# Performance work log

Measured on AMD Instinct MI355X. Metric: run time of the kernel, lower is better.

Reference implementation:

```python
import jax, jax.numpy as jnp
import numpy as np

B, S, D, H = 2, 4096, 1024, 16
HD = D // H
KCONV = 4


def _rmsnorm(x, scale, eps=1e-6):
    return x * jax.lax.rsqrt(jnp.mean(x * x, axis=-1, keepdims=True) + eps) * scale


def _l2norm(x, eps=1e-6):
    return x * jax.lax.rsqrt(jnp.sum(x * x, axis=-1, keepdims=True) + eps)


def _causal_dwconv_silu(x, w):
    # x: [B,S,D], w: [D,K] depthwise taps (tap K-1 multiplies x[t])
    k = w.shape[1]
    s = x.shape[1]
    xp = jnp.pad(x, ((0, 0), (k - 1, 0), (0, 0)))
    out = sum(xp[:, i:i + s, :] * w[:, i] for i in range(k))
    return jax.nn.silu(out)


def _p20_scan(x, decay_log, theta):
    # BLOCK_DIAGONAL_2 rotary-state linear recurrence: channels paired into
    # complex state, s_t = a * s_{t-1} + u_t with a = exp(-exp(decay_log) + i*theta).
    b, s, d = x.shape
    xc = x.reshape(b, s, d // 2, 2)
    u = jax.lax.complex(xc[..., 0], xc[..., 1])  # [B,S,D/2]
    a = jnp.exp(-jnp.exp(decay_log)) * jnp.exp(1j * theta)  # [D/2] complex, |a|<1

    def step(carry, u_t):
        st = carry * a + u_t
        return st, st

    _, ys = jax.lax.scan(step, jnp.zeros((b, d // 2), u.dtype), jnp.swapaxes(u, 0, 1))
    ys = jnp.swapaxes(ys, 0, 1)  # [B,S,D/2]
    return jnp.stack([ys.real, ys.imag], axis=-1).reshape(b, s, d)


def _gated_delta_rule(q, k, v, g, beta):
    # q,k,v: [B,S,H,Dh]; g,beta: [B,S,H]. State S: [B,H,K,V].
    scale = q.shape[-1] ** -0.5
    q = _l2norm(q)
    k = _l2norm(k)
    qt, kt, vt = (jnp.moveaxis(t, 1, 0) for t in (q, k, v))
    gt, bt = (jnp.moveaxis(t, 1, 0) for t in (g, beta))
    s0 = jnp.zeros((q.shape[0], q.shape[2], q.shape[3], v.shape[3]), v.dtype)

    def step(state, inp):
        q_t, k_t, v_t, g_t, b_t = inp
        state = state * jnp.exp(g_t)[..., None, None]
        v_err = (v_t - jnp.einsum('bhkv,bhk->bhv', state, k_t)) * b_t[..., None]
        state = state + jnp.einsum('bhk,bhv->bhkv', k_t, v_err)
        o_t = jnp.einsum('bhkv,bhk->bhv', state, q_t) * scale
        return state, o_t

    _, o = jax.lax.scan(step, s0, (qt, kt, vt, gt, bt))
    return jnp.moveaxis(o, 0, 1)  # [B,S,H,V]


def setup_inputs() -> dict:
    key = jax.random.key(0)
    ks = jax.random.split(key, 16)
    w = lambda k, shp, s=0.02: (jax.random.normal(k, shp, jnp.float32) * s)
    ctrl_out = 3 * D + 2 * H + D  # q,k,v,decay,beta,output_gate
    ctrl_b = jnp.concatenate([
        jnp.zeros((3 * D,), jnp.float32),
        jnp.full((H,), 1.5, jnp.float32),       # decay bias
        jnp.full((H,), -2.0, jnp.float32),      # beta bias
        jnp.full((D,), -1.5, jnp.float32),      # output gate bias
    ])
    # depthwise conv init: delta at last tap + small noise
    def conv_w(k):
        base = jnp.zeros((D, KCONV), jnp.float32).at[:, -1].set(1.0)
        return base + w(k, (D, KCONV), 0.02)
    return {
        'hidden': jax.random.normal(ks[0], (B, S, D), jnp.float32),
        'p20_decay_log': w(ks[1], (D // 2,), 1.0),
        'p20_theta': jax.random.uniform(ks[2], (D // 2,), jnp.float32, 0.0, 2.0 * np.pi),
        'ctrl_W': w(ks[3], (D, ctrl_out)),
        'ctrl_b': ctrl_b,
        'p20c_W': w(ks[4], (D, 3 * D), 0.001),  # 0.05-scaled init
        'qconv_w': conv_w(ks[5]),
        'kconv_w': conv_w(ks[6]),
        'vconv_w': conv_w(ks[7]),
        'mnorm_scale': jnp.ones((HD,), jnp.float32),
        'vnorm_scale': jnp.ones((D,), jnp.float32),
        'ramp_logit': jnp.full((D,), -4.595, jnp.float32),  # logit(0.01)
        'out_W': w(ks[8], (2 * D, D), 0.02),
        'out_b': jnp.zeros((D,), jnp.float32),
    }


def reference(hidden, p20_decay_log, p20_theta, ctrl_W, ctrl_b, p20c_W,
              qconv_w, kconv_w, vconv_w, mnorm_scale, vnorm_scale,
              ramp_logit, out_W, out_b):
    b, s, d = hidden.shape
    # P20 vector-state side channel
    p20_read = _p20_scan(hidden, p20_decay_log, p20_theta)
    normed_p20 = _rmsnorm(p20_read, vnorm_scale)
    p20_q, p20_k, p20_v = jnp.split(normed_p20 @ p20c_W, 3, axis=-1)
    ramp = jax.nn.sigmoid(ramp_logit)  # [D]
    # packed control projection
    ctrl = hidden @ ctrl_W + ctrl_b
    q_in, k_in, v_in, dec_in, beta_in, gate_in = jnp.split(
        ctrl, np.cumsum([d, d, d, H, H]).tolist(), axis=-1)
    # causal depthwise conv + SiLU
    q_in = _causal_dwconv_silu(q_in, qconv_w)
    k_in = _causal_dwconv_silu(k_in, kconv_w)
    v_in = _causal_dwconv_silu(v_in, vconv_w)
    # P20-conditioned heads
    queries = (q_in + ramp * p20_q).reshape(b, s, H, HD)
    keys = (k_in + ramp * p20_k).reshape(b, s, H, HD)
    values = (v_in + ramp * p20_v).reshape(b, s, H, HD)
    g = jax.nn.log_sigmoid(dec_in.astype(jnp.float32)).astype(hidden.dtype)  # [B,S,H]
    beta = jax.nn.sigmoid(beta_in)
    reads = _gated_delta_rule(queries, keys, values, g, beta)
    normed_reads = _rmsnorm(reads, mnorm_scale).reshape(b, s, d)
    fused = jnp.concatenate([normed_reads, normed_p20], axis=-1)
    projected = fused @ out_W + out_b
    return jax.nn.sigmoid(gate_in) * projected
```

## Files before the change

### kernel.cpp

```cpp
#include <hip/hip_runtime.h>
#include <hip/hip_bf16.h>
#include <stdint.h>

#define SEQ  4096
#define NH   16
#define HD   64

typedef __attribute__((ext_vector_type(8))) short bf16x8;
typedef __attribute__((ext_vector_type(4))) float f32x4;

__device__ __forceinline__ float bf2f(unsigned short u){
  union{unsigned u;float f;} v; v.u = ((unsigned)u)<<16; return v.f;
}
__device__ __forceinline__ unsigned short f2bf(float f){
  union{float f;unsigned u;} v; v.f=f;
  return (unsigned short)((v.u + 0x7fffu + ((v.u>>16)&1u))>>16);
}
__device__ __forceinline__ float sigm(float x){ return 1.f/(1.f+__expf(-x)); }
__device__ __forceinline__ f32x4 mfma16(bf16x8 a, bf16x8 b, f32x4 c){
  return __builtin_amdgcn_mfma_f32_16x16x32_bf16(a,b,c,0,0,0);
}
__device__ __forceinline__ void gll16(const void* g, void* l){
  __builtin_amdgcn_global_load_lds((const __attribute__((address_space(1))) void*)g,
                                   (__attribute__((address_space(3))) void*)l, 16, 0, 0);
}

__global__ void k_fill(float* __restrict__ p, float v, long n){
  long i = (long)blockIdx.x*blockDim.x + threadIdx.x;
  long stride = (long)gridDim.x*blockDim.x;
  for (; i<n; i+=stride) p[i] = v;
}

__global__ void k_cvt_bf16(const float* __restrict__ in, unsigned short* __restrict__ out){
  long i = ((long)blockIdx.x*256 + threadIdx.x)*4;
  float4 v = *(const float4*)(in+i);
  ushort4 o; o.x=f2bf(v.x); o.y=f2bf(v.y); o.z=f2bf(v.z); o.w=f2bf(v.w);
  *(ushort4*)(out+i) = o;
}

__global__ void k_transpose(const float* __restrict__ in, unsigned short* __restrict__ out,
                            int R, int Cin, int Cpad){
  __shared__ float t[32][33];
  int cb = blockIdx.x*32, rb = blockIdx.y*32;
  int tx = threadIdx.x & 31, ty = threadIdx.x >> 5;
  for (int k=0;k<32;k+=8){
    int r = rb+ty+k, c = cb+tx;
    t[ty+k][tx] = (c<Cin) ? in[(long)r*Cin + c] : 0.f;
  }
  __syncthreads();
  for (int k=0;k<32;k+=8){
    int c = cb+ty+k, r = rb+tx;
    if (c<Cpad) out[(long)c*R + r] = f2bf(t[tx][ty+k]);
  }
}

#define FOR16(F) F(0,0) F(0,1) F(0,2) F(0,3) F(1,0) F(1,1) F(1,2) F(1,3) \
                 F(2,0) F(2,1) F(2,2) F(2,3) F(3,0) F(3,1) F(3,2) F(3,3)
#define FOR4(F) F(0) F(1) F(2) F(3)
#define ACC(i,j) Ac##i##j

#define GEMM_CORE(A_,lda_,Bt_,ldb_,K_)                                         \
  __shared__ unsigned short Ab[3][4096];                                       \
  __shared__ unsigned short Bb[3][4096];                                       \
  const int tid=threadIdx.x, wid=tid>>6, l=tid&63;                             \
  const long m0=(long)blockIdx.y*128, n0=(long)blockIdx.x*128;                 \
  const int nk=(K_)>>5;                                                        \
  const int wm=(wid>>1)*64, wn=(wid&1)*64;                                     \
  const int srow0 = tid>>2;                                                    \
  const int schunk = (((tid&3) ^ ((tid>>2)&3))<<3);                            \
  const unsigned short* gA0 = (A_) + (m0+srow0)*(lda_) + schunk;               \
  const unsigned short* gA1 = (A_) + (m0+64+srow0)*(lda_) + schunk;            \
  const unsigned short* gB0 = (Bt_) + (n0+srow0)*(ldb_) + schunk;              \
  const unsigned short* gB1 = (Bt_) + (n0+64+srow0)*(ldb_) + schunk;           \
  const int ldst0 = tid*16, ldst1 = 4096 + tid*16;                             \
  f32x4 Ac00={0.f,0.f,0.f,0.f};                                                \
  f32x4 Ac01=Ac00,Ac02=Ac00,Ac03=Ac00,Ac10=Ac00,Ac11=Ac00,Ac12=Ac00,           \
        Ac13=Ac00,Ac20=Ac00,Ac21=Ac00,Ac22=Ac00,Ac23=Ac00,Ac30=Ac00,           \
        Ac31=Ac00,Ac32=Ac00,Ac33=Ac00;                                         \
  gll16(gA0, (char*)&Ab[0][0]+ldst0); gll16(gA1, (char*)&Ab[0][0]+ldst1);      \
  gll16(gB0, (char*)&Bb[0][0]+ldst0); gll16(gB1, (char*)&Bb[0][0]+ldst1);      \
  gA0+=32; gA1+=32; gB0+=32; gB1+=32;                                          \
  gll16(gA0, (char*)&Ab[1][0]+ldst0); gll16(gA1, (char*)&Ab[1][0]+ldst1);      \
  gll16(gB0, (char*)&Bb[1][0]+ldst0); gll16(gB1, (char*)&Bb[1][0]+ldst1);      \
  gA0+=32; gA1+=32; gB0+=32; gB1+=32;                                          \
  int rb=0, sb=2;                                                              \
  const int sxor = (l&3)<<4;                                                   \
  const int rao0 = (wm+(l&15))*64 + (((l>>4)<<4) ^ sxor);                      \
  const int rbo0 = (wn+(l&15))*64 + (((l>>4)<<4) ^ sxor);                      \
  for (int kt=0; kt<nk; ++kt){                                                 \
    if (kt+1<nk) { asm volatile("s_waitcnt vmcnt(4)" ::: "memory"); }          \
    else         { asm volatile("s_waitcnt vmcnt(0)" ::: "memory"); }          \
    __builtin_amdgcn_sched_barrier(0);                                         \
    __builtin_amdgcn_s_barrier();                                              \
    __builtin_amdgcn_sched_barrier(0);                                         \
    if (kt+2<nk){                                                              \
      gll16(gA0, (char*)&Ab[sb][0]+ldst0); gll16(gA1, (char*)&Ab[sb][0]+ldst1);\
      gll16(gB0, (char*)&Bb[sb][0]+ldst0); gll16(gB1, (char*)&Bb[sb][0]+ldst1);\
      gA0+=32; gA1+=32; gB0+=32; gB1+=32;                                      \
    }                                                                          \
    const char* Apt=(const char*)&Ab[rb][0];                                   \
    const char* Bpt=(const char*)&Bb[rb][0];                                   \
    bf16x8 af0=*(const bf16x8*)(Apt+rao0);      bf16x8 bf0=*(const bf16x8*)(Bpt+rbo0);      \
    bf16x8 af1=*(const bf16x8*)(Apt+rao0+1024); bf16x8 bf1=*(const bf16x8*)(Bpt+rbo0+1024); \
    bf16x8 af2=*(const bf16x8*)(Apt+rao0+2048); bf16x8 bf2=*(const bf16x8*)(Bpt+rbo0+2048); \
    bf16x8 af3=*(const bf16x8*)(Apt+rao0+3072); bf16x8 bf3=*(const bf16x8*)(Bpt+rbo0+3072); \
    __builtin_amdgcn_s_setprio(1);                                             \
    Ac00=mfma16(af0,bf0,Ac00); Ac01=mfma16(af0,bf1,Ac01);                      \
    Ac02=mfma16(af0,bf2,Ac02); Ac03=mfma16(af0,bf3,Ac03);                      \
    Ac10=mfma16(af1,bf0,Ac10); Ac11=mfma16(af1,bf1,Ac11);                      \
    Ac12=mfma16(af1,bf2,Ac12); Ac13=mfma16(af1,bf3,Ac13);                      \
    Ac20=mfma16(af2,bf0,Ac20); Ac21=mfma16(af2,bf1,Ac21);                      \
    Ac22=mfma16(af2,bf2,Ac22); Ac23=mfma16(af2,bf3,Ac23);                      \
    Ac30=mfma16(af3,bf0,Ac30); Ac31=mfma16(af3,bf1,Ac31);                      \
    Ac32=mfma16(af3,bf2,Ac32); Ac33=mfma16(af3,bf3,Ac33);                      \
    __builtin_amdgcn_s_setprio(0);                                             \
    rb = (rb==2)?0:rb+1; sb = (sb==2)?0:sb+1;                                  \
  }

__global__ __launch_bounds__(256,2) void k_gemm(
  const unsigned short* __restrict__ A, int lda,
  const unsigned short* __restrict__ Bt, int ldb,
  unsigned short* Cb, float* Cf, int ldc,
  int K, int Nvalid,
  const float* __restrict__ bias,
  const unsigned short* __restrict__ gate, int gld)
{
  GEMM_CORE(A, lda, Bt, ldb, K)
#define EPI_GEN(mi,ni) {                                                       \
  const int gn=(int)n0+wn+ni*16+(l&15);                                        \
  if (gn<Nvalid){                                                              \
    _Pragma("unroll") for(int r=0;r<4;r++){                                    \
      const long gm=m0+wm+mi*16+((l>>4)<<2)+r;                                 \
      float v=ACC(mi,ni)[r];                                                   \
      if(bias) v+=bias[gn];                                                    \
      if(gate) v*=bf2f(gate[gm*gld+gn]);                                       \
      if(Cb) Cb[gm*ldc+gn]=f2bf(v); else Cf[gm*ldc+gn]=v; } } }
  FOR16(EPI_GEN)
#undef EPI_GEN
}

__global__ __launch_bounds__(256,2) void k_gemm_ctrl(
  const unsigned short* __restrict__ A, int lda,
  const unsigned short* __restrict__ Bt, int ldb,
  unsigned short* __restrict__ ctrl,
  float* __restrict__ gbuf, float* __restrict__ bbuf,
  unsigned short* __restrict__ gateb,
  const float* __restrict__ bias)
{
  GEMM_CORE(A, lda, Bt, ldb, 1024)
#define EPI_CTRL(mi,ni) {                                                      \
  const int gn=(int)n0+wn+ni*16+(l&15);                                        \
  if (gn<4128){                                                                \
    const float bs=bias[gn];                                                   \
    _Pragma("unroll") for(int r=0;r<4;r++){                                    \
      const long gm=m0+wm+mi*16+((l>>4)<<2)+r;                                 \
      float v=ACC(mi,ni)[r]+bs;                                                \
      if (gn<3072)      ctrl[gm*3072+gn]=f2bf(v);                              \
      else if (gn<3088) gbuf[gm*16+(gn-3072)]=                                 \
                          (v>=0.f)?-log1pf(__expf(-v)):(v-log1pf(__expf(v)));  \
      else if (gn<3104) bbuf[gm*16+(gn-3088)]=sigm(v);                         \
      else              gateb[gm*1024+(gn-3104)]=f2bf(sigm(v)); } } }
  FOR16(EPI_CTRL)
#undef EPI_CTRL
}

__global__ __launch_bounds__(256,2) void k_gemm_qkv(
  const unsigned short* __restrict__ A, int lda,
  const unsigned short* __restrict__ Bt, int ldb,
  const float* __restrict__ ramp,
  unsigned short* __restrict__ Qb, unsigned short* __restrict__ Kb,
  unsigned short* __restrict__ Vb)
{
  GEMM_CORE(A, lda, Bt, ldb, 1024)
  const int seg = (int)((n0 + wn) >> 10);
  unsigned short* Ob = (seg==0)?Qb:((seg==1)?Kb:Vb);
  const int dc0=((int)n0+wn+0*16+(l&15))&1023; const float sr0=sigm(ramp[dc0]);
  const int dc1=((int)n0+wn+1*16+(l&15))&1023; const float sr1=sigm(ramp[dc1]);
  const int dc2=((int)n0+wn+2*16+(l&15))&1023; const float sr2=sigm(ramp[dc2]);
  const int dc3=((int)n0+wn+3*16+(l&15))&1023; const float sr3=sigm(ramp[dc3]);
#define EPI_QKV(mi) {                                                          \
  _Pragma("unroll") for(int r=0;r<4;r++){                                      \
    const long gm=m0+wm+mi*16+((l>>4)<<2)+r;                                   \
    float v0=bf2f(Ob[gm*1024+dc0])+sr0*ACC(mi,0)[r];                           \
    float v1=bf2f(Ob[gm*1024+dc1])+sr1*ACC(mi,1)[r];                           \
    float v2=bf2f(Ob[gm*1024+dc2])+sr2*ACC(mi,2)[r];                           \
    float v3=bf2f(Ob[gm*1024+dc3])+sr3*ACC(mi,3)[r];                           \
    if (seg<2){                                                                \
      float ss=v0*v0+v1*v1+v2*v2+v3*v3;                                        \
      ss+=__shfl_xor(ss,1); ss+=__shfl_xor(ss,2);                              \
      ss+=__shfl_xor(ss,4); ss+=__shfl_xor(ss,8);                              \
      float rs=rsqrtf(ss+1e-6f); v0*=rs; v1*=rs; v2*=rs; v3*=rs; }             \
    Ob[gm*1024+dc0]=f2bf(v0); Ob[gm*1024+dc1]=f2bf(v1);                        \
    Ob[gm*1024+dc2]=f2bf(v2); Ob[gm*1024+dc3]=f2bf(v3); } }
  FOR4(EPI_QKV)
#undef EPI_QKV
}

__global__ void k_scan1(const float* __restrict__ hidden, const float* __restrict__ dlog,
                        const float* __restrict__ theta, float2* __restrict__ finals){
  int idx = blockIdx.x*256 + threadIdx.x;
  int ch = idx & 511; int chunk = (idx>>9) & 63; int b = idx>>15;
  float e = __expf(dlog[ch]); float r = __expf(-e);
  float th = theta[ch]; float ar = r*__cosf(th), ai = r*__sinf(th);
  const float2* src = (const float2*)hidden + ((long)b*SEQ + chunk*64)*512 + ch;
  float sr=0.f, si=0.f;
  for (int j=0;j<64;j++){
    float2 u = src[(long)j*512];
    float nr = sr*ar - si*ai + u.x;
    si = sr*ai + si*ar + u.y; sr = nr;
  }
  finals[idx] = make_float2(sr,si);
}
__global__ void k_scan2(const float* __restrict__ dlog, const float* __restrict__ theta,
                        const float2* __restrict__ finals, float2* __restrict__ carry, int nb){
  int idx = blockIdx.x*256+threadIdx.x; if (idx>=nb*512) return;
  int ch = idx & 511, b = idx>>9;
  float e = __expf(dlog[ch]); float r64 = __expf(-64.f*e);
  float ang = fmodf(64.f*theta[ch], 6.2831853071795864f);
  float cr = r64*__cosf(ang), ci = r64*__sinf(ang);
  float pr=0.f, pi=0.f;
  for (int c=0;c<64;c++){
    long o = ((long)b*64 + c)*512 + ch;
    carry[o] = make_float2(pr,pi);
    float2 f = finals[o];
    float nr = pr*cr - pi*ci + f.x;
    pi = pr*ci + pi*cr + f.y; pr = nr;
  }
}
__global__ void k_scan3(const float* __restrict__ hidden, const float* __restrict__ dlog,
                        const float* __restrict__ theta, const float2* __restrict__ carry,
                        unsigned short* __restrict__ p20){
  int idx = blockIdx.x*256 + threadIdx.x;
  int ch = idx & 511; int chunk = (idx>>9) & 63; int b = idx>>15;
  float e = __expf(dlog[ch]); float r = __expf(-e);
  float th = theta[ch]; float ar = r*__cosf(th), ai = r*__sinf(th);
  long toff = (long)b*SEQ + chunk*64;
  const float2* src = (const float2*)hidden + toff*512 + ch;
  unsigned short* dst = p20 + toff*1024 + 2*ch;
  float2 c0 = carry[idx];
  float sr=c0.x, si=c0.y;
  for (int j=0;j<64;j++){
    float2 u = src[(long)j*512];
    float nr = sr*ar - si*ai + u.x;
    si = sr*ai + si*ar + u.y; sr = nr;
    ushort2 o; o.x=f2bf(sr); o.y=f2bf(si);
    *(ushort2*)(dst + (long)j*1024) = o;
  }
}

__global__ __launch_bounds__(256) void k_rms_p20(const unsigned short* __restrict__ p20,
                        const float* __restrict__ vns, unsigned short* __restrict__ fused){
  long t = blockIdx.x;
  int d = threadIdx.x*4;
  ushort4 xu = *(const ushort4*)(p20 + t*1024 + d);
  float x0=bf2f(xu.x), x1=bf2f(xu.y), x2=bf2f(xu.z), x3=bf2f(xu.w);
  float ss = x0*x0 + x1*x1 + x2*x2 + x3*x3;
  for (int o=1;o<64;o<<=1) ss += __shfl_xor(ss, o);
  __shared__ float red[4];
  if ((threadIdx.x&63)==0) red[threadIdx.x>>6] = ss;
  __syncthreads();
  ss = red[0]+red[1]+red[2]+red[3];
  float rs = rsqrtf(ss*(1.f/1024.f) + 1e-6f);
  float4 s4 = *(const float4*)(vns + d);
  ushort4 o4;
  o4.x = f2bf(x0*rs*s4.x); o4.y = f2bf(x1*rs*s4.y);
  o4.z = f2bf(x2*rs*s4.z); o4.w = f2bf(x3*rs*s4.w);
  *(ushort4*)(fused + t*2048 + 1024 + d) = o4;
}

__global__ __launch_bounds__(256) void k_conv(const unsigned short* __restrict__ ctrl,
   const float* __restrict__ qw, const float* __restrict__ kw, const float* __restrict__ vw,
   unsigned short* __restrict__ Q, unsigned short* __restrict__ Kb, unsigned short* __restrict__ Vb){
  __shared__ unsigned short pan[19][256];
  int panel = blockIdx.x;
  int tb = blockIdx.y;
  int b = tb >> 8; int s0 = (tb & 255) * 16;
  int seg = panel >> 2; int d = (panel & 3)*256 + threadIdx.x;
  int c0 = panel*256;
  long base = (long)b*SEQ*3072;
  for (int rr=0; rr<19; rr++){
    int s = s0 - 3 + rr;
    pan[rr][threadIdx.x] = (s>=0) ? ctrl[base + (long)s*3072 + c0 + threadIdx.x] : (unsigned short)0;
  }
  __syncthreads();
  const float* cw = (seg==0)?qw:((seg==1)?kw:vw);
  float w0=cw[d*4], w1=cw[d*4+1], w2=cw[d*4+2], w3=cw[d*4+3];
  unsigned short* Ob = (seg==0)?Q:((seg==1)?Kb:Vb);
  for (int tk=0; tk<16; tk++){
    long t = (long)b*SEQ + s0 + tk;
    float x = bf2f(pan[tk][threadIdx.x])*w0 + bf2f(pan[tk+1][threadIdx.x])*w1
            + bf2f(pan[tk+2][threadIdx.x])*w2 + bf2f(pan[tk+3][threadIdx.x])*w3;
    x = x * sigm(x);
    Ob[t*1024 + d] = f2bf(x);
  }
}

__global__ __launch_bounds__(64,2) void k_phase1(
    const unsigned short* __restrict__ Kg, const unsigned short* __restrict__ Vg,
    const float* __restrict__ g, const float* __restrict__ beta,
    unsigned short* __restrict__ uvT, unsigned short* __restrict__ Wrm,
    unsigned short* __restrict__ Mc, unsigned short* __restrict__ BcT){
  __shared__ unsigned short Kc[64*64];
  __shared__ unsigned short Vc[64*64];
  __shared__ float Af[64*64];
  __shared__ unsigned short uTb[64*72];
  __shared__ unsigned short wTb[64*72];
  __shared__ float Gs[64], betl[64], bgam[64], decC[64];

  int bid = blockIdx.x; int bh = bid>>6, c = bid&63;
  int blocal = bh>>4, h = bh&15;
  long t0 = (long)blocal*SEQ + c*64;
  int l = threadIdx.x;
  long cbase = (long)bid*4096;

  float G = g[(t0+l)*16 + h];
  for (int o=1;o<64;o<<=1){ float n = __shfl_up(G,o); if (l>=o) G += n; }
  float bl = beta[(t0+l)*16+h];
  Gs[l]=G; betl[l]=bl; bgam[l]=bl*__expf(G);
  float G63 = __shfl(G,63);
  decC[l] = __expf(G63 - G);
  float GamC = __expf(G63);

  for (int it=0; it<8; it++){
    int bo = it*1024 + l*16;
    int row = bo>>7, bib = bo&127;
    int sb2 = bib ^ ((row&7)<<4);
    gll16(Kg + (t0+row)*1024 + h*64 + (sb2>>1),  (char*)Kc + bo);
    gll16(Vg + (t0+row)*1024 + h*64 + (bib>>1), (char*)Vc + bo);
  }
  __syncthreads();

  bf16x8 kf[2][4];
  {
    int rr = l&15;
    #pragma unroll
    for (int t=0;t<4;t++)
      #pragma unroll
      for (int h2=0;h2<2;h2++){
        int row = t*16 + rr;
        int byt = row*128 + ((h2*64 + (l>>4)*16) ^ ((row&7)<<4));
        kf[h2][t] = *(const bf16x8*)((const char*)Kc + byt);
      }
  }
  #pragma unroll
  for (int ti=0;ti<4;ti++){
    #pragma unroll
    for (int tj=0;tj<4;tj++){
      f32x4 a = {0.f,0.f,0.f,0.f};
      a = mfma16(kf[0][ti], kf[0][tj], a);
      a = mfma16(kf[1][ti], kf[1][tj], a);
      int j = tj*16 + (l&15);
      float Gj = Gs[j];
      #pragma unroll
      for (int r=0;r<4;r++){
        int i = ti*16 + ((l>>4)<<2) + r;
        Af[i*64+j] = (j<i) ? betl[i]*a[r]*__expf(Gs[i]-Gj) : 0.f;
      }
    }
  }
  __syncthreads();

  float ww[64];
  {
    float uu[64];
    #pragma unroll
    for (int i=0;i<64;i++){
      float ua = betl[i]*bf2f(Vc[i*64 + l]);
      float wa = bgam[i]*bf2f(*(const unsigned short*)((const char*)Kc + i*128 + ((2*l) ^ ((i&7)<<4))));
      #pragma unroll
      for (int j=0;j<i;j++){
        float av = Af[i*64+j];
        ua -= av*uu[j];
        wa -= av*ww[j];
      }
      uu[i] = ua; ww[i] = wa;
    }
    #pragma unroll
    for (int i=0;i<64;i+=4){
      short4 pu, pw;
      pu.x=(short)f2bf(uu[i]);   pu.y=(short)f2bf(uu[i+1]);
      pu.z=(short)f2bf(uu[i+2]); pu.w=(short)f2bf(uu[i+3]);
      pw.x=(short)f2bf(ww[i]);   pw.y=(short)f2bf(ww[i+1]);
      pw.z=(short)f2bf(ww[i+2]); pw.w=(short)f2bf(ww[i+3]);
      *(short4*)&uTb[l*72+i] = pu;
      *(short4*)&wTb[l*72+i] = pw;
    }
  }
  __syncthreads();

  unsigned short* KTp = (unsigned short*)Af;
  for (int j=0;j<64;j++){
    float kv = bf2f(*(const unsigned short*)((const char*)Kc + j*128 + ((2*l) ^ ((j&7)<<4))));
    *(unsigned short*)((char*)KTp + l*128 + ((2*j) ^ ((l&7)<<4))) = f2bf(decC[j]*kv);
  }
  __syncthreads();

  auto ldfragKT = [&](int t, int h2)->bf16x8{
    int row = t*16 + (l&15);
    int byt = row*128 + ((h2*64 + (l>>4)*16) ^ ((row&7)<<4));
    return *(const bf16x8*)((const char*)KTp + byt);
  };
  auto ldfrag72 = [&](const unsigned short* base, int nrow, int h2)->bf16x8{
    return *(const bf16x8*)(base + nrow*72 + h2*32 + ((l>>4)<<3));
  };

  #pragma unroll
  for (int to=0; to<4; to++){
    bf16x8 a0 = ldfragKT(to,0), a1 = ldfragKT(to,1);
    #pragma unroll
    for (int tn=0; tn<4; tn++){
      f32x4 accv = {0.f,0.f,0.f,0.f};
      accv = mfma16(a0, ldfrag72(wTb, tn*16+(l&15), 0), accv);
      accv = mfma16(a1, ldfrag72(wTb, tn*16+(l&15), 1), accv);
      int col = tn*16 + (l&15);
      #pragma unroll
      for (int r=0;r<4;r++){
        int row = to*16 + ((l>>4)<<2) + r;
        Mc[cbase + row*64 + col] = f2bf(((row==col)? GamC : 0.f) - accv[r]);
      }
    }
    #pragma unroll
    for (int tv=0; tv<4; tv++){
      f32x4 accv = {0.f,0.f,0.f,0.f};
      accv = mfma16(a0, ldfrag72(uTb, tv*16+(l&15), 0), accv);
      accv = mfma16(a1, ldfrag72(uTb, tv*16+(l&15), 1), accv);
      int v = tv*16 + (l&15);
      int k0 = to*16 + ((l>>4)<<2);
      short4 p;
      p.x=(short)f2bf(accv[0]); p.y=(short)f2bf(accv[1]);
      p.z=(short)f2bf(accv[2]); p.w=(short)f2bf(accv[3]);
      *(short4*)&BcT[cbase + v*64 + k0] = p;
    }
  }

  #pragma unroll
  for (int rr=0; rr<64; rr++){
    uvT[cbase + rr*64 + l] = uTb[rr*72 + l];
    Wrm[cbase + rr*64 + l] = f2bf(ww[rr]);
  }
}

__global__ __launch_bounds__(64,2) void k_phase2(
    const unsigned short* __restrict__ Mc, const unsigned short* __restrict__ BcT,
    unsigned short* __restrict__ Sst){
  __shared__ unsigned short ST[64*64];
  int bh = blockIdx.x; int l = threadIdx.x;
  f32x4 acc[4][4];
  { f32x4 z = {0.f,0.f,0.f,0.f};
    #pragma unroll
    for (int i=0;i<4;i++)
      #pragma unroll
      for (int j=0;j<4;j++) acc[i][j]=z; }

  for (int c=0;c<64;c++){
    long cbase = ((long)bh*64 + c)*4096;
    #pragma unroll
    for (int ti=0;ti<4;ti++){
      #pragma unroll
      for (int tj=0;tj<4;tj++){
        int v = tj*16 + (l&15);
        int kd0 = ti*16 + ((l>>4)<<2);
        short4 p;
        p.x=(short)f2bf(acc[ti][tj][0]); p.y=(short)f2bf(acc[ti][tj][1]);
        p.z=(short)f2bf(acc[ti][tj][2]); p.w=(short)f2bf(acc[ti][tj][3]);
        *(short4*)&Sst[cbase + v*64 + kd0] = p;
        *(short4*)((char*)ST + v*128 + ((2*kd0) ^ ((v&7)<<4))) = p;
      }
    }
    __syncthreads();
    bf16x8 mf[2][4];
    #pragma unroll
    for (int ti=0;ti<4;ti++){
      int row = ti*16 + (l&15);
      mf[0][ti] = *(const bf16x8*)(Mc + cbase + row*64 + (l>>4)*8);
      mf[1][ti] = *(const bf16x8*)(Mc + cbase + row*64 + 32 + (l>>4)*8);
    }
    #pragma unroll
    for (int ti=0;ti<4;ti++)
      #pragma unroll
      for (int tj=0;tj<4;tj++){
        short4 bv = *(const short4*)&BcT[cbase + (long)(tj*16+(l&15))*64 + ti*16 + ((l>>4)<<2)];
        acc[ti][tj][0]=bf2f((unsigned short)bv.x); acc[ti][tj][1]=bf2f((unsigned short)bv.y);
        acc[ti][tj][2]=bf2f((unsigned short)bv.z); acc[ti][tj][3]=bf2f((unsigned short)bv.w);
      }
    bf16x8 sf[2][4];
    #pragma unroll
    for (int tj=0;tj<4;tj++){
      int v = tj*16 + (l&15);
      sf[0][tj] = *(const bf16x8*)((const char*)ST + v*128 + (((l>>4)*16) ^ ((v&7)<<4)));
      sf[1][tj] = *(const bf16x8*)((const char*)ST + v*128 + ((64+(l>>4)*16) ^ ((v&7)<<4)));
    }
    #pragma unroll
    for (int ti=0;ti<4;ti++)
      #pragma unroll
      for (int tj=0;tj<4;tj++){
        acc[ti][tj] = mfma16(mf[0][ti], sf[0][tj], acc[ti][tj]);
        acc[ti][tj] = mfma16(mf[1][ti], sf[1][tj], acc[ti][tj]);
      }
    __syncthreads();
  }
}

__global__ __launch_bounds__(64,2) void k_phase3(
  const unsigned short* __restrict__ Qg, const unsigned short* __restrict__ Kg,
  const float* __restrict__ g,
  const unsigned short* __restrict__ uvT, const unsigned short* __restrict__ Wrm,
  const unsigned short* __restrict__ Sst, const float* __restrict__ mns,
  unsigned short* __restrict__ fused){
  __shared__ unsigned short ST[64*64];
  __shared__ unsigned short QKl[64*64];
  __shared__ unsigned short uT[64*64];
  __shared__ float Gs[64];
  int bid = blockIdx.x; int bh = bid>>6, c = bid&63;
  int blocal = bh>>4, h = bh&15; long t0 = (long)blocal*SEQ + c*64;
  long cbase = (long)bid*4096;
  int l = threadIdx.x;

  float G = g[(t0+l)*16+h];
  for (int o=1;o<64;o<<=1){ float n=__shfl_up(G,o); if(l>=o) G+=n; }
  Gs[l]=G;

  #pragma unroll
  for (int it=0; it<16; it++){
    int flat = it*256 + l*4;
    int v = flat>>6, kd0 = flat&63;
    short4 s4 = *(const short4*)&Sst[cbase + flat];
    *(short4*)((char*)ST + v*128 + ((2*kd0) ^ ((v&7)<<4))) = s4;
  }
  __syncthreads();

  bf16x8 qf[2][4], kfr[2][4], sf[2][4];
  #pragma unroll
  for (int t=0;t<4;t++){
    long tr = t0 + t*16 + (l&15);
    qf[0][t]  = *(const bf16x8*)(Qg + tr*1024 + h*64 + (l>>4)*8);
    qf[1][t]  = *(const bf16x8*)(Qg + tr*1024 + h*64 + 32 + (l>>4)*8);
    kfr[0][t] = *(const bf16x8*)(Kg + tr*1024 + h*64 + (l>>4)*8);
    kfr[1][t] = *(const bf16x8*)(Kg + tr*1024 + h*64 + 32 + (l>>4)*8);
    int v = t*16 + (l&15);
    sf[0][t] = *(const bf16x8*)((const char*)ST + v*128 + (((l>>4)*16) ^ ((v&7)<<4)));
    sf[1][t] = *(const bf16x8*)((const char*)ST + v*128 + ((64+(l>>4)*16) ^ ((v&7)<<4)));
  }

  f32x4 qs[4][4];
  #pragma unroll
  for (int ti=0;ti<4;ti++)
    #pragma unroll
    for (int tj=0;tj<4;tj++){
      f32x4 a = {0.f,0.f,0.f,0.f};
      a = mfma16(qf[0][ti], sf[0][tj], a);
      a = mfma16(qf[1][ti], sf[1][tj], a);
      qs[ti][tj] = a;
    }

  #pragma unroll
  for (int ti=0;ti<4;ti++)
    #pragma unroll
    for (int tj=0;tj<4;tj++){
      f32x4 a = {0.f,0.f,0.f,0.f};
      a = mfma16(qf[0][ti], kfr[0][tj], a);
      a = mfma16(qf[1][ti], kfr[1][tj], a);
      int j = tj*16 + (l&15);
      float Gj = Gs[j];
      #pragma unroll
      for (int r=0;r<4;r++){
        int i = ti*16 + ((l>>4)<<2) + r;
        float v = (j<=i)? a[r]*__expf(Gs[i]-Gj) : 0.f;
        *(unsigned short*)((char*)QKl + i*128 + ((2*j) ^ ((i&7)<<4))) = f2bf(v);
      }
    }

  #pragma unroll
  for (int ti=0; ti<4; ti++){
    int irow = ti*16 + (l&15);
    bf16x8 w0 = *(const bf16x8*)(Wrm + cbase + irow*64 + (l>>4)*8);
    bf16x8 w1 = *(const bf16x8*)(Wrm + cbase + irow*64 + 32 + (l>>4)*8);
    #pragma unroll
    for (int tj=0; tj<4; tj++){
      f32x4 a = {0.f,0.f,0.f,0.f};
      a = mfma16(w0, sf[0][tj], a);
      a = mfma16(w1, sf[1][tj], a);
      int v = tj*16 + (l&15);
      int i0 = ti*16 + ((l>>4)<<2);
      short4 uv4 = *(const short4*)(uvT + cbase + (long)v*64 + i0);
      short4 p;
      p.x=(short)f2bf(bf2f((unsigned short)uv4.x) - a[0]);
      p.y=(short)f2bf(bf2f((unsigned short)uv4.y) - a[1]);
      p.z=(short)f2bf(bf2f((unsigned short)uv4.z) - a[2]);
      p.w=(short)f2bf(bf2f((unsigned short)uv4.w) - a[3]);
      *(short4*)((char*)uT + v*128 + ((2*i0) ^ ((v&7)<<4))) = p;
    }
  }
  __syncthreads();

  float mscale[4];
  #pragma unroll
  for (int tj=0;tj<4;tj++) mscale[tj] = mns[tj*16 + (l&15)];
  #pragma unroll
  for (int ti=0; ti<4; ti++){
    int row = ti*16 + (l&15);
    bf16x8 qk0 = *(const bf16x8*)((const char*)QKl + row*128 + (((l>>4)*16) ^ ((row&7)<<4)));
    bf16x8 qk1 = *(const bf16x8*)((const char*)QKl + row*128 + ((64+(l>>4)*16) ^ ((row&7)<<4)));
    #pragma unroll
    for (int tj=0; tj<4; tj++){
      int v = tj*16 + (l&15);
      bf16x8 u0 = *(const bf16x8*)((const char*)uT + v*128 + (((l>>4)*16) ^ ((v&7)<<4)));
      bf16x8 u1 = *(const bf16x8*)((const char*)uT + v*128 + ((64+(l>>4)*16) ^ ((v&7)<<4)));
      f32x4 a;
      #pragma unroll
      for (int r=0;r<4;r++){
        float gam = __expf(Gs[ti*16 + ((l>>4)<<2) + r]);
        a[r] = qs[ti][tj][r]*gam;
      }
      a = mfma16(qk0,u0,a);
      a = mfma16(qk1,u1,a);
      qs[ti][tj] = a;
    }
  }
  #pragma unroll
  for (int ti=0; ti<4; ti++){
    #pragma unroll
    for (int r=0; r<4; r++){
      float ss = 0.f;
      #pragma unroll
      for (int tj=0;tj<4;tj++){ float v = qs[ti][tj][r]*0.125f; ss += v*v; }
      ss += __shfl_xor(ss,1); ss += __shfl_xor(ss,2); ss += __shfl_xor(ss,4); ss += __shfl_xor(ss,8);
      float rs = rsqrtf(ss*(1.f/64.f) + 1e-6f);
      long t = t0 + ti*16 + ((l>>4)<<2) + r;
      #pragma unroll
      for (int tj=0;tj<4;tj++){
        float on = qs[ti][tj][r]*0.125f*rs*mscale[tj];
        fused[t*2048 + h*64 + tj*16 + (l&15)] = f2bf(on);
      }
    }
  }
}

extern "C" void kernel_launch(void* const* d_in, const int* in_sizes, int n_in,
                              void* d_out, int out_size, void* d_ws, size_t ws_size,
                              hipStream_t stream){
  (void)in_sizes; (void)n_in;
  const float* hidden = (const float*)d_in[0];
  const float* dlog   = (const float*)d_in[1];
  const float* theta  = (const float*)d_in[2];
  const float* ctrlW  = (const float*)d_in[3];
  const float* ctrlb  = (const float*)d_in[4];
  const float* p20cW  = (const float*)d_in[5];
  const float* qw     = (const float*)d_in[6];
  const float* kw     = (const float*)d_in[7];
  const float* vw     = (const float*)d_in[8];
  const float* mns    = (const float*)d_in[9];
  const float* vns    = (const float*)d_in[10];
  const float* ramp   = (const float*)d_in[11];
  const float* outW   = (const float*)d_in[12];
  const float* outb   = (const float*)d_in[13];
  float* out = (float*)d_out;

  struct Bufs {
    unsigned short *ctrl, *uvT, *Wrm, *Mc;
    unsigned short *Qb, *Kb, *Vb, *fused;
    unsigned short *E_hid, *E_p20, *BcT;
    unsigned short *Sst, *gateb, *ctrlWT, *p20WT, *outWT;
    float2 *finals, *carry; float *gbuf, *bbuf;
    size_t need;
  };
  auto mk = [&](size_t NT)->Bufs{
    Bufs B; size_t off=0;
    auto tk=[&](size_t n)->char*{ char* p=(char*)d_ws+off; off += (n+255)&~(size_t)255; return p; };
    char* Rctrl = tk(NT*3072*2);
    B.ctrl=(unsigned short*)Rctrl;
    B.uvT=(unsigned short*)Rctrl; B.Wrm=B.uvT + NT*1024; B.Mc=B.Wrm + NT*1024;
    char* Rqkv = tk(NT*1024*2*3);
    B.Qb=(unsigned short*)Rqkv; B.Kb=B.Qb+NT*1024; B.Vb=B.Kb+NT*1024;
    B.fused=(unsigned short*)tk(NT*2048*2);
    char* RE = tk(NT*1024*2);
    B.E_hid=(unsigned short*)RE; B.E_p20=(unsigned short*)RE; B.BcT=(unsigned short*)RE;
    B.Sst=(unsigned short*)tk(NT*1024*2);
    B.gateb=(unsigned short*)tk(NT*1024*2);
    B.ctrlWT=(unsigned short*)tk((size_t)4224*1024*2);
    B.p20WT=(unsigned short*)tk((size_t)3072*1024*2);
    B.outWT=(unsigned short*)tk((size_t)1024*2048*2);
    B.finals=(float2*)tk(NT*64);
    B.carry=(float2*)tk(NT*64);
    B.gbuf=(float*)tk(NT*16*4);
    B.bbuf=(float*)tk(NT*16*4);
    B.need=off;
    return B;
  };

  Bufs Bf = mk(8192);
  Bufs Bh = mk(4096);
  Bufs B; size_t NT; int nb;
  if      (Bf.need <= ws_size){ B=Bf; NT=8192; nb=2; }
  else if (Bh.need <= ws_size){ B=Bh; NT=4096; nb=1; }
  else {
    k_fill<<<2048,256,0,stream>>>(out, (float)((double)ws_size), (long)out_size);
    return;
  }

  k_transpose<<<dim3(132,32),256,0,stream>>>(ctrlW, B.ctrlWT, 1024, 4128, 4224);
  k_transpose<<<dim3(96,32), 256,0,stream>>>(p20cW, B.p20WT, 1024, 3072, 3072);
  k_transpose<<<dim3(32,64), 256,0,stream>>>(outW,  B.outWT, 2048, 1024, 1024);

  for (int b0=0; b0<2; b0+=nb){
    const float* hidb = hidden + (size_t)b0*SEQ*1024;
    float* outp = out + (size_t)b0*SEQ*1024;
    k_cvt_bf16<<<(int)NT,256,0,stream>>>(hidb, B.E_hid);
    k_gemm_ctrl<<<dim3(33,NT/128),256,0,stream>>>(B.E_hid,1024, B.ctrlWT,1024,
                                                  B.ctrl, B.gbuf, B.bbuf, B.gateb, ctrlb);
    k_scan1<<<nb*128,256,0,stream>>>(hidb,dlog,theta,B.finals);
    k_scan2<<<nb*2, 256,0,stream>>>(dlog,theta,B.finals,B.carry,nb);
    k_scan3<<<nb*128,256,0,stream>>>(hidb,dlog,theta,B.carry,B.E_p20);
    k_rms_p20<<<(int)NT,256,0,stream>>>(B.E_p20,vns,B.fused);
    k_conv<<<dim3(12,NT/16),256,0,stream>>>(B.ctrl,qw,kw,vw,B.Qb,B.Kb,B.Vb);
    k_gemm_qkv<<<dim3(24,NT/128),256,0,stream>>>(B.fused+1024,2048, B.p20WT,1024,
                                                 ramp, B.Qb,B.Kb,B.Vb);
    k_phase1<<<(int)(NT/4),64,0,stream>>>(B.Kb,B.Vb,B.gbuf,B.bbuf,B.uvT,B.Wrm,B.Mc,B.BcT);
    k_phase2<<<nb*16,64,0,stream>>>(B.Mc,B.BcT,B.Sst);
    k_phase3<<<(int)(NT/4),64,0,stream>>>(B.Qb,B.Kb,B.gbuf,B.uvT,B.Wrm,B.Sst,mns,B.fused);
    k_gemm<<<dim3(8,NT/128),256,0,stream>>>(B.fused,2048, B.outWT,2048,
                                            nullptr,outp,1024, 2048,1024, outb, B.gateb,1024);
  }
}
```

Baseline: 581.9 us.

## Split phase2 state recurrence across value columns; remap GEMM blocks and swizzle

The chunk-state recurrence kernel now launches four workgroups per batch-head, each owning a 16-column slice of the value dimension, instead of one workgroup holding the whole 64x64 state. Each block still reloads the full M chunk matrix. This raises parallelism for a kernel that previously ran only nb*16 single-wave blocks. Separately, the GEMM core remaps flat block indices so that consecutive blocks are interleaved across groups of eight. It also changes the LDS XOR swizzle to use different lane bits, which targets bank conflicts and cache locality but alters the layout the stores and reads must agree on.

```diff
diff --git a/kernel.cpp b/kernel.cpp
--- a/kernel.cpp
+++ b/kernel.cpp
@@ -63,11 +63,15 @@
   __shared__ unsigned short Ab[3][4096];                                       \
   __shared__ unsigned short Bb[3][4096];                                       \
   const int tid=threadIdx.x, wid=tid>>6, l=tid&63;                             \
-  const long m0=(long)blockIdx.y*128, n0=(long)blockIdx.x*128;                 \
+  const int nbx=(int)gridDim.x;                                               \
+  const int nwg=nbx*(int)gridDim.y;                                           \
+  int flat=(int)blockIdx.y*nbx+(int)blockIdx.x;                                \
+  flat=(flat&7)*(nwg>>3)+(flat>>3);                                           \
+  const long m0=(long)(flat/nbx)*128, n0=(long)(flat%nbx)*128;                 \
   const int nk=(K_)>>5;                                                        \
   const int wm=(wid>>1)*64, wn=(wid&1)*64;                                     \
   const int srow0 = tid>>2;                                                    \
-  const int schunk = (((tid&3) ^ ((tid>>2)&3))<<3);                            \
+  const int schunk = (((tid&3) ^ ((tid>>4)&3))<<3);                            \
   const unsigned short* gA0 = (A_) + (m0+srow0)*(lda_) + schunk;               \
   const unsigned short* gA1 = (A_) + (m0+64+srow0)*(lda_) + schunk;            \
   const unsigned short* gB0 = (Bt_) + (n0+srow0)*(ldb_) + schunk;              \
@@ -84,7 +88,7 @@
   gll16(gB0, (char*)&Bb[1][0]+ldst0); gll16(gB1, (char*)&Bb[1][0]+ldst1);      \
   gA0+=32; gA1+=32; gB0+=32; gB1+=32;                                          \
   int rb=0, sb=2;                                                              \
-  const int sxor = (l&3)<<4;                                                   \
+  const int sxor = ((l>>2)&3)<<4;                                              \
   const int rao0 = (wm+(l&15))*64 + (((l>>4)<<4) ^ sxor);                      \
   const int rbo0 = (wn+(l&15))*64 + (((l>>4)<<4) ^ sxor);                      \
   for (int kt=0; kt<nk; ++kt){                                                 \
@@ -443,60 +447,43 @@
 __global__ __launch_bounds__(64,2) void k_phase2(
     const unsigned short* __restrict__ Mc, const unsigned short* __restrict__ BcT,
     unsigned short* __restrict__ Sst){
-  __shared__ unsigned short ST[64*64];
-  int bh = blockIdx.x; int l = threadIdx.x;
-  f32x4 acc[4][4];
-  { f32x4 z = {0.f,0.f,0.f,0.f};
-    #pragma unroll
-    for (int i=0;i<4;i++)
-      #pragma unroll
-      for (int j=0;j<4;j++) acc[i][j]=z; }
-
+  __shared__ unsigned short ST[16*64];
+  const int bh = blockIdx.x>>2, vq = blockIdx.x&3;
+  const int l = threadIdx.x;
+  const int vloc = l&15;
+  const int v = vq*16 + vloc;
+  f32x4 Ac0={0.f,0.f,0.f,0.f};
+  f32x4 Ac1=Ac0, Ac2=Ac0, Ac3=Ac0;
   for (int c=0;c<64;c++){
     long cbase = ((long)bh*64 + c)*4096;
-    #pragma unroll
-    for (int ti=0;ti<4;ti++){
-      #pragma unroll
-      for (int tj=0;tj<4;tj++){
-        int v = tj*16 + (l&15);
-        int kd0 = ti*16 + ((l>>4)<<2);
-        short4 p;
-        p.x=(short)f2bf(acc[ti][tj][0]); p.y=(short)f2bf(acc[ti][tj][1]);
-        p.z=(short)f2bf(acc[ti][tj][2]); p.w=(short)f2bf(acc[ti][tj][3]);
-        *(short4*)&Sst[cbase + v*64 + kd0] = p;
-        *(short4*)((char*)ST + v*128 + ((2*kd0) ^ ((v&7)<<4))) = p;
-      }
-    }
+#define P2ST(ti,A) { int kd0 = ti*16 + ((l>>4)<<2); short4 p;                  \
+      p.x=(short)f2bf(A[0]); p.y=(short)f2bf(A[1]);                            \
+      p.z=(short)f2bf(A[2]); p.w=(short)f2bf(A[3]);                            \
+      *(short4*)&Sst[cbase + (long)v*64 + kd0] = p;                            \
+      *(short4*)((char*)ST + vloc*128 + ((2*kd0) ^ ((vloc&7)<<4))) = p; }
+    P2ST(0,Ac0) P2ST(1,Ac1) P2ST(2,Ac2) P2ST(3,Ac3)
+#undef P2ST
     __syncthreads();
-    bf16x8 mf[2][4];
-    #pragma unroll
-    for (int ti=0;ti<4;ti++){
-      int row = ti*16 + (l&15);
-      mf[0][ti] = *(const bf16x8*)(Mc + cbase + row*64 + (l>>4)*8);
-      mf[1][ti] = *(const bf16x8*)(Mc + cbase + row*64 + 32 + (l>>4)*8);
-    }
-    #pragma unroll
-    for (int ti=0;ti<4;ti++)
-      #pragma unroll
-      for (int tj=0;tj<4;tj++){
-        short4 bv = *(const short4*)&BcT[cbase + (long)(tj*16+(l&15))*64 + ti*16 + ((l>>4)<<2)];
-        acc[ti][tj][0]=bf2f((unsigned short)bv.x); acc[ti][tj][1]=bf2f((unsigned short)bv.y);
-        acc[ti][tj][2]=bf2f((unsigned short)bv.z); acc[ti][tj][3]=bf2f((unsigned short)bv.w);
-      }
-    bf16x8 sf[2][4];
-    #pragma unroll
-    for (int tj=0;tj<4;tj++){
-      int v = tj*16 + (l&15);
-      sf[0][tj] = *(const bf16x8*)((const char*)ST + v*128 + (((l>>4)*16) ^ ((v&7)<<4)));
-      sf[1][tj] = *(const bf16x8*)((const char*)ST + v*128 + ((64+(l>>4)*16) ^ ((v&7)<<4)));
-    }
-    #pragma unroll
-    for (int ti=0;ti<4;ti++)
-      #pragma unroll
-      for (int tj=0;tj<4;tj++){
-        acc[ti][tj] = mfma16(mf[0][ti], sf[0][tj], acc[ti][tj]);
-        acc[ti][tj] = mfma16(mf[1][ti], sf[1][tj], acc[ti][tj]);
-      }
+    const unsigned short* Mp = Mc + cbase;
+    bf16x8 m0a = *(const bf16x8*)(Mp + ( 0+(l&15))*64 + (l>>4)*8);
+    bf16x8 m0b = *(const bf16x8*)(Mp + ( 0+(l&15))*64 + 32 + (l>>4)*8);
+    bf16x8 m1a = *(const bf16x8*)(Mp + (16+(l&15))*64 + (l>>4)*8);
+    bf16x8 m1b = *(const bf16x8*)(Mp + (16+(l&15))*64 + 32 + (l>>4)*8);
+    bf16x8 m2a = *(const bf16x8*)(Mp + (32+(l&15))*64 + (l>>4)*8);
+    bf16x8 m2b = *(const bf16x8*)(Mp + (32+(l&15))*64 + 32 + (l>>4)*8);
+    bf16x8 m3a = *(const bf16x8*)(Mp + (48+(l&15))*64 + (l>>4)*8);
+    bf16x8 m3b = *(const bf16x8*)(Mp + (48+(l&15))*64 + 32 + (l>>4)*8);
+#define P2LD(ti,A) { short4 bv = *(const short4*)&BcT[cbase + (long)v*64 + ti*16 + ((l>>4)<<2)]; \
+      A[0]=bf2f((unsigned short)bv.x); A[1]=bf2f((unsigned short)bv.y);        \
+      A[2]=bf2f((unsigned short)bv.z); A[3]=bf2f((unsigned short)bv.w); }
+    P2LD(0,Ac0) P2LD(1,Ac1) P2LD(2,Ac2) P2LD(3,Ac3)
+#undef P2LD
+    bf16x8 sfa = *(const bf16x8*)((const char*)ST + vloc*128 + (((l>>4)*16) ^ ((vloc&7)<<4)));
+    bf16x8 sfb = *(const bf16x8*)((const char*)ST + vloc*128 + ((64+(l>>4)*16) ^ ((vloc&7)<<4)));
+    Ac0 = mfma16(m0a, sfa, Ac0); Ac0 = mfma16(m0b, sfb, Ac0);
+    Ac1 = mfma16(m1a, sfa, Ac1); Ac1 = mfma16(m1b, sfb, Ac1);
+    Ac2 = mfma16(m2a, sfa, Ac2); Ac2 = mfma16(m2b, sfb, Ac2);
+    Ac3 = mfma16(m3a, sfa, Ac3); Ac3 = mfma16(m3b, sfb, Ac3);
     __syncthreads();
   }
 }
@@ -716,7 +703,7 @@
     k_gemm_qkv<<<dim3(24,NT/128),256,0,stream>>>(B.fused+1024,2048, B.p20WT,1024,
                                                  ramp, B.Qb,B.Kb,B.Vb);
     k_phase1<<<(int)(NT/4),64,0,stream>>>(B.Kb,B.Vb,B.gbuf,B.bbuf,B.uvT,B.Wrm,B.Mc,B.BcT);
-    k_phase2<<<nb*16,64,0,stream>>>(B.Mc,B.BcT,B.Sst);
+    k_phase2<<<nb*64,64,0,stream>>>(B.Mc,B.BcT,B.Sst);
     k_phase3<<<(int)(NT/4),64,0,stream>>>(B.Qb,B.Kb,B.gbuf,B.uvT,B.Wrm,B.Sst,mns,B.fused);
     k_gemm<<<dim3(8,NT/128),256,0,stream>>>(B.fused,2048, B.outWT,2048,
                                             nullptr,outp,1024, 2048,1024, outb, B.gateb,1024);
```

After: 543.6 us. 1.07x faster.
